# Kernel optimization log

Measured on AMD Instinct MI355X. Metric: run time of the kernel, lower is better.

The kernel has to match this reference:

```python
import jax, jax.numpy as jnp
import numpy as np
from jax import lax

NEAR, FAR = 0.05, 20.0


def _quat_to_mat(q):
    # q: [..., 4] in xyzw order (scipy from_quat convention); normalizes like scipy
    q = q / jnp.linalg.norm(q, axis=-1, keepdims=True)
    x, y, z, w = q[..., 0], q[..., 1], q[..., 2], q[..., 3]
    r00 = 1 - 2 * (y * y + z * z); r01 = 2 * (x * y - z * w); r02 = 2 * (x * z + y * w)
    r10 = 2 * (x * y + z * w); r11 = 1 - 2 * (x * x + z * z); r12 = 2 * (y * z - x * w)
    r20 = 2 * (x * z - y * w); r21 = 2 * (y * z + x * w); r22 = 1 - 2 * (x * x + y * y)
    return jnp.stack([jnp.stack([r00, r01, r02], -1),
                      jnp.stack([r10, r11, r12], -1),
                      jnp.stack([r20, r21, r22], -1)], -2)


def _mat_to_quat_wxyz(m):
    # Vectorized Shepperd method matching scipy R.from_matrix().as_quat(scalar_first=True)
    m00, m01, m02 = m[..., 0, 0], m[..., 0, 1], m[..., 0, 2]
    m10, m11, m12 = m[..., 1, 0], m[..., 1, 1], m[..., 1, 2]
    m20, m21, m22 = m[..., 2, 0], m[..., 2, 1], m[..., 2, 2]
    tr = m00 + m11 + m22
    q0 = jnp.stack([1 + tr, m21 - m12, m02 - m20, m10 - m01], -1)          # trace branch
    q1 = jnp.stack([m21 - m12, 1 + m00 - m11 - m22, m01 + m10, m02 + m20], -1)  # x branch
    q2 = jnp.stack([m02 - m20, m01 + m10, 1 + m11 - m00 - m22, m12 + m21], -1)  # y branch
    q3 = jnp.stack([m10 - m01, m02 + m20, m12 + m21, 1 + m22 - m00 - m11], -1)  # z branch
    choice = jnp.argmax(jnp.stack([m00, m11, m22, tr], -1), axis=-1)[..., None]
    q = jnp.where(choice == 0, q1, jnp.where(choice == 1, q2, jnp.where(choice == 2, q3, q0)))
    return q / jnp.linalg.norm(q, axis=-1, keepdims=True)


def setup_inputs() -> dict:
    key = jax.random.key(0)
    k1, k2, k3 = jax.random.split(key, 3)
    b, v, c, h, w = 1, 8, 14, 480, 640
    raw = jax.random.normal(k1, (b, v, c, h, w), dtype=jnp.float32)
    # valid SE(3) extrinsics: random unit quaternion -> rotation, random translation
    q = jax.random.normal(k2, (b, v, 4), dtype=jnp.float32)
    Rm = _quat_to_mat(q)
    t = jax.random.normal(k3, (b, v, 3), dtype=jnp.float32)
    ext = jnp.zeros((b, v, 4, 4), jnp.float32)
    ext = ext.at[..., :3, :3].set(Rm).at[..., :3, 3].set(t).at[..., 3, 3].set(1.0)
    intr = jnp.array([[500.0, 0.0, 320.0], [0.0, 500.0, 240.0], [0.0, 0.0, 1.0]], jnp.float32)
    intr = jnp.broadcast_to(intr, (b, v, 3, 3))
    return {"raw_gaussians": raw, "extrinsics": ext, "intrinsics": intr}


def reference(raw_gaussians, extrinsics, intrinsics):
    b, v, c, h, w = raw_gaussians.shape
    raw = jnp.transpose(raw_gaussians, (0, 1, 3, 4, 2))  # b v h w c
    rgb = raw[..., 0:3]; disp = raw[..., 3:4]; opacity = raw[..., 4:5]
    scales = raw[..., 5:8]; rotations = raw[..., 8:12]; xy_offset = raw[..., 12:14]
    # pixel grid, indexing='xy' over (w, h) -> (h, w, 2) with [...,0]=x, [...,1]=y
    xx, yy = jnp.meshgrid(jnp.arange(w, dtype=raw.dtype), jnp.arange(h, dtype=raw.dtype))
    pixel = jnp.stack([xx, yy], -1)
    coords = pixel + (jax.nn.sigmoid(xy_offset) - 0.5)                # b v h w 2
    coords = jnp.concatenate([coords, jnp.ones_like(coords[..., :1])], -1)
    inv_intr = jnp.linalg.inv(intrinsics)                             # b v 3 3
    dirs = jnp.einsum('bvij,bvhwj->bvhwi', inv_intr, coords)
    dirs = dirs / jnp.linalg.norm(dirs, axis=-1, keepdims=True)
    dirs = jnp.concatenate([dirs, jnp.zeros_like(dirs[..., :1])], -1)  # homogeneous dir
    dirs = jnp.einsum('bvij,bvhwj->bvhwi', extrinsics, dirs)           # world-frame rays
    origins = extrinsics[:, :, None, None, :, 3]                       # b v 1 1 4
    depths = 1.0 / (jax.nn.sigmoid(disp) * (1.0 / NEAR - 1.0 / FAR) + 1.0 / FAR)
    means = origins + dirs * depths                                    # b v h w 4
    # scale multiplier: sum of entries of inv(K[:2,:2]) per view
    mult = jnp.linalg.inv(intrinsics[..., :2, :2]).sum(axis=(-1, -2))  # b v
    scales = jax.nn.softplus(scales) * mult[:, :, None, None, None]
    rot = rotations / (jnp.linalg.norm(rotations, axis=-1, keepdims=True) + 1e-8)
    rot = lax.stop_gradient(rot)  # original detaches before scipy conversion
    cam_m = _quat_to_mat(rot)                                          # b v h w 3 3
    src = lax.stop_gradient(extrinsics)[:, :, None, None, :3, :3]
    world_q = _mat_to_quat_wxyz(src @ cam_m)                           # b v h w 4 (wxyz)
    opacity = jax.nn.sigmoid(opacity)
    rgb = jax.nn.softplus(rgb)
    # pack: means(4) rgb(3) opacity(1) scale(3) rotation(4) -> (v, h, w, 15) for batch 0
    out = jnp.concatenate([means, rgb, opacity, scales, world_q], axis=-1)[0]
    return out
```

## Files before the change

kernel.cpp:

```cpp
#include <hip/hip_runtime.h>
#include <math.h>

#define NV 8
#define NC 14
#define NH 480
#define NW 640
#define HW (NH * NW)
#define NPIX (NV * HW)
#define OC 15
#define BLK 256

#define LOG2E 1.44269504088896340736f
#define LN2   0.69314718055994530942f

__device__ __forceinline__ float fexp2_(float x) {
#if __has_builtin(__builtin_amdgcn_exp2f)
    return __builtin_amdgcn_exp2f(x);
#else
    return exp2f(x);
#endif
}
__device__ __forceinline__ float flog2_(float x) {
#if __has_builtin(__builtin_amdgcn_logf)
    return __builtin_amdgcn_logf(x);
#else
    return log2f(x);
#endif
}
__device__ __forceinline__ float frcp_(float x) {
#if __has_builtin(__builtin_amdgcn_rcpf)
    return __builtin_amdgcn_rcpf(x);
#else
    return 1.0f / x;
#endif
}
__device__ __forceinline__ float frsq_(float x) {
#if __has_builtin(__builtin_amdgcn_rsqf)
    return __builtin_amdgcn_rsqf(x);
#else
    return rsqrtf(x);
#endif
}

__device__ __forceinline__ float sigmoidf_(float x) {
    return frcp_(1.0f + fexp2_(-x * LOG2E));
}
__device__ __forceinline__ float softplusf_(float x) {
    return fmaxf(x, 0.0f) + LN2 * flog2_(1.0f + fexp2_(-fabsf(x) * LOG2E));
}

__global__ __launch_bounds__(BLK) void DecoderSplatting_kernel(
    const float* __restrict__ raw,
    const float* __restrict__ ext,
    const float* __restrict__ intr,
    float* __restrict__ out)
{
    __shared__ __align__(16) float sout[BLK * OC];

    const int tid = threadIdx.x;
    const int blockStart = blockIdx.x * BLK;
    const int v = blockStart / HW;
    const int pin = blockStart - v * HW + tid;
    const int py = pin / NW;
    const int px = pin - py * NW;

    const float* E = ext + v * 16;
    const float* K = intr + v * 9;
    const float a00 = K[0], a01 = K[1], a02 = K[2];
    const float a10 = K[3], a11 = K[4], a12 = K[5];
    const float a20 = K[6], a21 = K[7], a22 = K[8];
    const float c00 = a11 * a22 - a12 * a21;
    const float c01 = a12 * a20 - a10 * a22;
    const float c02 = a10 * a21 - a11 * a20;
    const float invdet = 1.0f / (a00 * c00 + a01 * c01 + a02 * c02);
    const float i00 = c00 * invdet;
    const float i01 = (a02 * a21 - a01 * a22) * invdet;
    const float i02 = (a01 * a12 - a02 * a11) * invdet;
    const float i10 = c01 * invdet;
    const float i11 = (a00 * a22 - a02 * a20) * invdet;
    const float i12 = (a02 * a10 - a00 * a12) * invdet;
    const float i20 = c02 * invdet;
    const float i21 = (a01 * a20 - a00 * a21) * invdet;
    const float i22 = (a00 * a11 - a01 * a10) * invdet;
    const float mult = (a00 + a11 - a01 - a10) / (a00 * a11 - a01 * a10);

    const float* rp = raw + (size_t)v * NC * HW + pin;
    float ch[NC];
#pragma unroll
    for (int c = 0; c < NC; ++c) ch[c] = rp[(size_t)c * HW];

    const float cx = (float)px + sigmoidf_(ch[12]) - 0.5f;
    const float cy = (float)py + sigmoidf_(ch[13]) - 0.5f;
    float dx = i00 * cx + i01 * cy + i02;
    float dy = i10 * cx + i11 * cy + i12;
    float dz = i20 * cx + i21 * cy + i22;
    const float dinv = frsq_(dx * dx + dy * dy + dz * dz);
    dx *= dinv; dy *= dinv; dz *= dinv;

    const float depth = frcp_(sigmoidf_(ch[3]) * 19.95f + 0.05f);
    const float m0 = E[3]  + (E[0]  * dx + E[1]  * dy + E[2]  * dz) * depth;
    const float m1 = E[7]  + (E[4]  * dx + E[5]  * dy + E[6]  * dz) * depth;
    const float m2 = E[11] + (E[8]  * dx + E[9]  * dy + E[10] * dz) * depth;
    const float m3 = E[15] + (E[12] * dx + E[13] * dy + E[14] * dz) * depth;

    const float r0 = softplusf_(ch[0]);
    const float r1 = softplusf_(ch[1]);
    const float r2 = softplusf_(ch[2]);
    const float op = sigmoidf_(ch[4]);
    const float s0 = softplusf_(ch[5]) * mult;
    const float s1 = softplusf_(ch[6]) * mult;
    const float s2 = softplusf_(ch[7]) * mult;

    float qx = ch[8], qy = ch[9], qz = ch[10], qw = ch[11];
    const float qinv = frsq_(qx * qx + qy * qy + qz * qz + qw * qw);
    qx *= qinv; qy *= qinv; qz *= qinv; qw *= qinv;

    const float b00 = 1.0f - 2.0f * (qy * qy + qz * qz);
    const float b01 = 2.0f * (qx * qy - qz * qw);
    const float b02 = 2.0f * (qx * qz + qy * qw);
    const float b10 = 2.0f * (qx * qy + qz * qw);
    const float b11 = 1.0f - 2.0f * (qx * qx + qz * qz);
    const float b12 = 2.0f * (qy * qz - qx * qw);
    const float b20 = 2.0f * (qx * qz - qy * qw);
    const float b21 = 2.0f * (qy * qz + qx * qw);
    const float b22 = 1.0f - 2.0f * (qx * qx + qy * qy);

    const float M00 = E[0] * b00 + E[1] * b10 + E[2] * b20;
    const float M01 = E[0] * b01 + E[1] * b11 + E[2] * b21;
    const float M02 = E[0] * b02 + E[1] * b12 + E[2] * b22;
    const float M10 = E[4] * b00 + E[5] * b10 + E[6] * b20;
    const float M11 = E[4] * b01 + E[5] * b11 + E[6] * b21;
    const float M12 = E[4] * b02 + E[5] * b12 + E[6] * b22;
    const float M20 = E[8] * b00 + E[9] * b10 + E[10] * b20;
    const float M21 = E[8] * b01 + E[9] * b11 + E[10] * b21;
    const float M22 = E[8] * b02 + E[9] * b12 + E[10] * b22;

    const float tr = M00 + M11 + M22;
    int choice = 0;
    float best = M00;
    if (M11 > best) { best = M11; choice = 1; }
    if (M22 > best) { best = M22; choice = 2; }
    if (tr  > best) { best = tr;  choice = 3; }

    float w0, w1, w2, w3;
    if (choice == 0) {
        w0 = M21 - M12;
        w1 = 1.0f + M00 - M11 - M22;
        w2 = M01 + M10;
        w3 = M02 + M20;
    } else if (choice == 1) {
        w0 = M02 - M20;
        w1 = M01 + M10;
        w2 = 1.0f + M11 - M00 - M22;
        w3 = M12 + M21;
    } else if (choice == 2) {
        w0 = M10 - M01;
        w1 = M02 + M20;
        w2 = M12 + M21;
        w3 = 1.0f + M22 - M00 - M11;
    } else {
        w0 = 1.0f + tr;
        w1 = M21 - M12;
        w2 = M02 - M20;
        w3 = M10 - M01;
    }
    const float winv = frsq_(w0 * w0 + w1 * w1 + w2 * w2 + w3 * w3);
    w0 *= winv; w1 *= winv; w2 *= winv; w3 *= winv;

    float* so = sout + tid * OC;
    so[0]  = m0;  so[1]  = m1;  so[2]  = m2;  so[3]  = m3;
    so[4]  = r0;  so[5]  = r1;  so[6]  = r2;
    so[7]  = op;
    so[8]  = s0;  so[9]  = s1;  so[10] = s2;
    so[11] = w0;  so[12] = w1;  so[13] = w2;  so[14] = w3;

    __syncthreads();

    const float4* s4 = (const float4*)sout;
    float4* o4 = (float4*)(out + (size_t)blockStart * OC);
#pragma unroll
    for (int j = 0; j < (BLK * OC) / 4; j += BLK) {
        const int idx = j + tid;
        if (idx < (BLK * OC) / 4) o4[idx] = s4[idx];
    }
}

extern "C" void kernel_launch(void* const* d_in, const int* in_sizes, int n_in,
                              void* d_out, int out_size, void* d_ws, size_t ws_size,
                              hipStream_t stream) {
    const float* raw  = (const float*)d_in[0];
    const float* ext  = (const float*)d_in[1];
    const float* intr = (const float*)d_in[2];
    float* out = (float*)d_out;

    dim3 grid(NPIX / BLK);
    dim3 block(BLK);
    DecoderSplatting_kernel<<<grid, block, 0, stream>>>(raw, ext, intr, out);
}
```

Measured before the change: 248.9 us.

## Process four pixels per thread with float4 loads and direct register stores

Each thread now handles four consecutive pixels. Every channel is read with one float4 load, and each thread writes its 60 contiguous output floats as 15 float4 stores straight from registers. This drops the shared-memory staging buffer and the block barrier, and amortises per-thread setup such as the intrinsic inverse and extrinsic loads. In exchange, the global stores are strided across lanes (240 bytes per thread), which hurts write coalescing, and register pressure rises.

After: 286.4 us. 1.15x slower.

```diff
diff --git a/kernel.cpp b/kernel.cpp
--- a/kernel.cpp
+++ b/kernel.cpp
@@ -9,6 +9,10 @@
 #define NPIX (NV * HW)
 #define OC 15
 #define BLK 256
+#define PPT 4
+#define PPB (BLK * PPT)
+#define BPV (HW / PPB)
+#define NB  (NPIX / PPB)
 
 #define LOG2E 1.44269504088896340736f
 #define LN2   0.69314718055994530942f
@@ -49,20 +53,17 @@
     return fmaxf(x, 0.0f) + LN2 * flog2_(1.0f + fexp2_(-fabsf(x) * LOG2E));
 }
 
-__global__ __launch_bounds__(BLK) void DecoderSplatting_kernel(
+__global__ __launch_bounds__(BLK, 4) void DecoderSplatting_kernel(
     const float* __restrict__ raw,
     const float* __restrict__ ext,
     const float* __restrict__ intr,
     float* __restrict__ out)
 {
-    __shared__ __align__(16) float sout[BLK * OC];
-
     const int tid = threadIdx.x;
-    const int blockStart = blockIdx.x * BLK;
-    const int v = blockStart / HW;
-    const int pin = blockStart - v * HW + tid;
-    const int py = pin / NW;
-    const int px = pin - py * NW;
+    const int v = blockIdx.x / BPV;
+    const int pin0 = (blockIdx.x - v * BPV) * PPB + tid * PPT;
+    const int py  = pin0 / NW;
+    const int px0 = pin0 - py * NW;
 
     const float* E = ext + v * 16;
     const float* K = intr + v * 9;
@@ -84,105 +85,103 @@
     const float i22 = (a00 * a11 - a01 * a10) * invdet;
     const float mult = (a00 + a11 - a01 - a10) / (a00 * a11 - a01 * a10);
 
-    const float* rp = raw + (size_t)v * NC * HW + pin;
-    float ch[NC];
+    const float e0 = E[0],  e1 = E[1],  e2 = E[2],  e3 = E[3];
+    const float e4 = E[4],  e5 = E[5],  e6 = E[6],  e7 = E[7];
+    const float e8 = E[8],  e9 = E[9],  e10 = E[10], e11 = E[11];
+    const float e12 = E[12], e13 = E[13], e14 = E[14], e15 = E[15];
+
+    const float* base = raw + (size_t)v * NC * HW;
+    float4 ch4[NC];
 #pragma unroll
-    for (int c = 0; c < NC; ++c) ch[c] = rp[(size_t)c * HW];
+    for (int c = 0; c < NC; ++c)
+        ch4[c] = *(const float4*)(base + (size_t)c * HW + pin0);
 
-    const float cx = (float)px + sigmoidf_(ch[12]) - 0.5f;
-    const float cy = (float)py + sigmoidf_(ch[13]) - 0.5f;
-    float dx = i00 * cx + i01 * cy + i02;
-    float dy = i10 * cx + i11 * cy + i12;
-    float dz = i20 * cx + i21 * cy + i22;
-    const float dinv = frsq_(dx * dx + dy * dy + dz * dz);
-    dx *= dinv; dy *= dinv; dz *= dinv;
+    float ob[PPT * OC];
 
-    const float depth = frcp_(sigmoidf_(ch[3]) * 19.95f + 0.05f);
-    const float m0 = E[3]  + (E[0]  * dx + E[1]  * dy + E[2]  * dz) * depth;
-    const float m1 = E[7]  + (E[4]  * dx + E[5]  * dy + E[6]  * dz) * depth;
-    const float m2 = E[11] + (E[8]  * dx + E[9]  * dy + E[10] * dz) * depth;
-    const float m3 = E[15] + (E[12] * dx + E[13] * dy + E[14] * dz) * depth;
+#pragma unroll
+    for (int p = 0; p < PPT; ++p) {
+        float ch[NC];
+#pragma unroll
+        for (int c = 0; c < NC; ++c)
+            ch[c] = (p == 0) ? ch4[c].x : (p == 1) ? ch4[c].y : (p == 2) ? ch4[c].z : ch4[c].w;
 
-    const float r0 = softplusf_(ch[0]);
-    const float r1 = softplusf_(ch[1]);
-    const float r2 = softplusf_(ch[2]);
-    const float op = sigmoidf_(ch[4]);
-    const float s0 = softplusf_(ch[5]) * mult;
-    const float s1 = softplusf_(ch[6]) * mult;
-    const float s2 = softplusf_(ch[7]) * mult;
+        const float cx = (float)(px0 + p) + sigmoidf_(ch[12]) - 0.5f;
+        const float cy = (float)py + sigmoidf_(ch[13]) - 0.5f;
+        float dx = i00 * cx + i01 * cy + i02;
+        float dy = i10 * cx + i11 * cy + i12;
+        float dz = i20 * cx + i21 * cy + i22;
+        const float dinv = frsq_(dx * dx + dy * dy + dz * dz);
+        dx *= dinv; dy *= dinv; dz *= dinv;
 
-    float qx = ch[8], qy = ch[9], qz = ch[10], qw = ch[11];
-    const float qinv = frsq_(qx * qx + qy * qy + qz * qz + qw * qw);
-    qx *= qinv; qy *= qinv; qz *= qinv; qw *= qinv;
+        const float depth = frcp_(sigmoidf_(ch[3]) * 19.95f + 0.05f);
+        const float m0 = e3  + (e0  * dx + e1  * dy + e2  * dz) * depth;
+        const float m1 = e7  + (e4  * dx + e5  * dy + e6  * dz) * depth;
+        const float m2 = e11 + (e8  * dx + e9  * dy + e10 * dz) * depth;
+        const float m3 = e15 + (e12 * dx + e13 * dy + e14 * dz) * depth;
 
-    const float b00 = 1.0f - 2.0f * (qy * qy + qz * qz);
-    const float b01 = 2.0f * (qx * qy - qz * qw);
-    const float b02 = 2.0f * (qx * qz + qy * qw);
-    const float b10 = 2.0f * (qx * qy + qz * qw);
-    const float b11 = 1.0f - 2.0f * (qx * qx + qz * qz);
-    const float b12 = 2.0f * (qy * qz - qx * qw);
-    const float b20 = 2.0f * (qx * qz - qy * qw);
-    const float b21 = 2.0f * (qy * qz + qx * qw);
-    const float b22 = 1.0f - 2.0f * (qx * qx + qy * qy);
+        const float r0 = softplusf_(ch[0]);
+        const float r1 = softplusf_(ch[1]);
+        const float r2 = softplusf_(ch[2]);
+        const float op = sigmoidf_(ch[4]);
+        const float s0 = softplusf_(ch[5]) * mult;
+        const float s1 = softplusf_(ch[6]) * mult;
+        const float s2 = softplusf_(ch[7]) * mult;
 
-    const float M00 = E[0] * b00 + E[1] * b10 + E[2] * b20;
-    const float M01 = E[0] * b01 + E[1] * b11 + E[2] * b21;
-    const float M02 = E[0] * b02 + E[1] * b12 + E[2] * b22;
-    const float M10 = E[4] * b00 + E[5] * b10 + E[6] * b20;
-    const float M11 = E[4] * b01 + E[5] * b11 + E[6] * b21;
-    const float M12 = E[4] * b02 + E[5] * b12 + E[6] * b22;
-    const float M20 = E[8] * b00 + E[9] * b10 + E[10] * b20;
-    const float M21 = E[8] * b01 + E[9] * b11 + E[10] * b21;
-    const float M22 = E[8] * b02 + E[9] * b12 + E[10] * b22;
+        float qx = ch[8], qy = ch[9], qz = ch[10], qw = ch[11];
+        const float qinv = frsq_(qx * qx + qy * qy + qz * qz + qw * qw);
+        qx *= qinv; qy *= qinv; qz *= qinv; qw *= qinv;
 
-    const float tr = M00 + M11 + M22;
-    int choice = 0;
-    float best = M00;
-    if (M11 > best) { best = M11; choice = 1; }
-    if (M22 > best) { best = M22; choice = 2; }
-    if (tr  > best) { best = tr;  choice = 3; }
+        const float b00 = 1.0f - 2.0f * (qy * qy + qz * qz);
+        const float b01 = 2.0f * (qx * qy - qz * qw);
+        const float b02 = 2.0f * (qx * qz + qy * qw);
+        const float b10 = 2.0f * (qx * qy + qz * qw);
+        const float b11 = 1.0f - 2.0f * (qx * qx + qz * qz);
+        const float b12 = 2.0f * (qy * qz - qx * qw);
+        const float b20 = 2.0f * (qx * qz - qy * qw);
+        const float b21 = 2.0f * (qy * qz + qx * qw);
+        const float b22 = 1.0f - 2.0f * (qx * qx + qy * qy);
 
-    float w0, w1, w2, w3;
-    if (choice == 0) {
-        w0 = M21 - M12;
-        w1 = 1.0f + M00 - M11 - M22;
-        w2 = M01 + M10;
-        w3 = M02 + M20;
-    } else if (choice == 1) {
-        w0 = M02 - M20;
-        w1 = M01 + M10;
-        w2 = 1.0f + M11 - M00 - M22;
-        w3 = M12 + M21;
-    } else if (choice == 2) {
-        w0 = M10 - M01;
-        w1 = M02 + M20;
-        w2 = M12 + M21;
-        w3 = 1.0f + M22 - M00 - M11;
-    } else {
-        w0 = 1.0f + tr;
-        w1 = M21 - M12;
-        w2 = M02 - M20;
-        w3 = M10 - M01;
+        const float M00 = e0 * b00 + e1 * b10 + e2 * b20;
+        const float M01 = e0 * b01 + e1 * b11 + e2 * b21;
+        const float M02 = e0 * b02 + e1 * b12 + e2 * b22;
+        const float M10 = e4 * b00 + e5 * b10 + e6 * b20;
+        const float M11 = e4 * b01 + e5 * b11 + e6 * b21;
+        const float M12 = e4 * b02 + e5 * b12 + e6 * b22;
+        const float M20 = e8 * b00 + e9 * b10 + e10 * b20;
+        const float M21 = e8 * b01 + e9 * b11 + e10 * b21;
+        const float M22 = e8 * b02 + e9 * b12 + e10 * b22;
+
+        const float tr = M00 + M11 + M22;
+        int choice = 0;
+        float best = M00;
+        if (M11 > best) { best = M11; choice = 1; }
+        if (M22 > best) { best = M22; choice = 2; }
+        if (tr  > best) { best = tr;  choice = 3; }
+
+        float w0, w1, w2, w3;
+        if (choice == 0) {
+            w0 = M21 - M12; w1 = 1.0f + M00 - M11 - M22; w2 = M01 + M10; w3 = M02 + M20;
+        } else if (choice == 1) {
+            w0 = M02 - M20; w1 = M01 + M10; w2 = 1.0f + M11 - M00 - M22; w3 = M12 + M21;
+        } else if (choice == 2) {
+            w0 = M10 - M01; w1 = M02 + M20; w2 = M12 + M21; w3 = 1.0f + M22 - M00 - M11;
+        } else {
+            w0 = 1.0f + tr; w1 = M21 - M12; w2 = M02 - M20; w3 = M10 - M01;
+        }
+        const float winv = frsq_(w0 * w0 + w1 * w1 + w2 * w2 + w3 * w3);
+
+        float* o = ob + p * OC;
+        o[0]  = m0;  o[1]  = m1;  o[2]  = m2;  o[3]  = m3;
+        o[4]  = r0;  o[5]  = r1;  o[6]  = r2;
+        o[7]  = op;
+        o[8]  = s0;  o[9]  = s1;  o[10] = s2;
+        o[11] = w0 * winv; o[12] = w1 * winv; o[13] = w2 * winv; o[14] = w3 * winv;
     }
-    const float winv = frsq_(w0 * w0 + w1 * w1 + w2 * w2 + w3 * w3);
-    w0 *= winv; w1 *= winv; w2 *= winv; w3 *= winv;
 
-    float* so = sout + tid * OC;
-    so[0]  = m0;  so[1]  = m1;  so[2]  = m2;  so[3]  = m3;
-    so[4]  = r0;  so[5]  = r1;  so[6]  = r2;
-    so[7]  = op;
-    so[8]  = s0;  so[9]  = s1;  so[10] = s2;
-    so[11] = w0;  so[12] = w1;  so[13] = w2;  so[14] = w3;
-
-    __syncthreads();
-
-    const float4* s4 = (const float4*)sout;
-    float4* o4 = (float4*)(out + (size_t)blockStart * OC);
+    float4* o4 = (float4*)(out + (size_t)(v * HW + pin0) * OC);
 #pragma unroll
-    for (int j = 0; j < (BLK * OC) / 4; j += BLK) {
-        const int idx = j + tid;
-        if (idx < (BLK * OC) / 4) o4[idx] = s4[idx];
-    }
+    for (int j = 0; j < (PPT * OC) / 4; ++j)
+        o4[j] = *(const float4*)(ob + 4 * j);
 }
 
 extern "C" void kernel_launch(void* const* d_in, const int* in_sizes, int n_in,
@@ -193,7 +192,5 @@
     const float* intr = (const float*)d_in[2];
     float* out = (float*)d_out;
 
-    dim3 grid(NPIX / BLK);
-    dim3 block(BLK);
-    DecoderSplatting_kernel<<<grid, block, 0, stream>>>(raw, ext, intr, out);
+    DecoderSplatting_kernel<<<dim3(NB), dim3(BLK), 0, stream>>>(raw, ext, intr, out);
 }
```
